# Kernel optimization log

Measured on AMD Instinct MI355X. Metric: run time of the kernel, lower is better.

The kernel has to match this reference:

```python
import jax, jax.numpy as jnp
import numpy as np

NEG_INF = -jnp.inf


def setup_inputs() -> dict:
    key = jax.random.key(0)
    ks = jax.random.split(key, 20)
    B, N, M = 8, 1024, 128
    F_OP, F_MA, F_E, OUT, HID = 64, 64, 16, 64, 128
    inp = {
        "x": jax.random.normal(ks[0], (B, N, F_OP), dtype=jnp.float32),
        "y": jax.random.normal(ks[1], (B, M, F_MA), dtype=jnp.float32),
        "z": jax.random.normal(ks[2], (B, N, M, F_E), dtype=jnp.float32),
        "op_adj_in": jax.random.randint(ks[3], (B, N, N), 0, 2, dtype=jnp.int32),
        "ma_adj_in": jax.random.randint(ks[4], (B, N, N), 0, 2, dtype=jnp.int32),
        "op_ma_adj": jax.random.randint(ks[5], (B, N, M), 0, 2, dtype=jnp.int32),
        # learned parameters
        "weight_op": jax.random.normal(ks[6], (F_OP, OUT), dtype=jnp.float32) * 0.1,
        "weight_ma": jax.random.normal(ks[7], (F_MA, OUT), dtype=jnp.float32) * 0.1,
        "weight_edge": jax.random.normal(ks[8], (F_E, OUT), dtype=jnp.float32) * 0.1,
        "attention_op": jax.random.normal(ks[9], (1, 2 * OUT), dtype=jnp.float32) * 0.1,
        "attention_ma": jax.random.normal(ks[10], (1, 3 * OUT), dtype=jnp.float32) * 0.1,
        "w1": jax.random.normal(ks[11], (2 * OUT, HID), dtype=jnp.float32) * 0.1,
        "b1": jnp.zeros((HID,), dtype=jnp.float32),
        "w2": jax.random.normal(ks[12], (HID, HID), dtype=jnp.float32) * 0.1,
        "b2": jnp.zeros((HID,), dtype=jnp.float32),
        "wo": jax.random.normal(ks[13], (HID, OUT), dtype=jnp.float32) * 0.1,
        "bo": jnp.zeros((OUT,), dtype=jnp.float32),
    }
    return inp


def reference(x, y, z, op_adj_in, ma_adj_in, op_ma_adj,
              weight_op, weight_ma, weight_edge, attention_op, attention_ma,
              w1, b1, w2, b2, wo, bo):
    OUT = weight_op.shape[1]
    h = jnp.einsum('bni,io->bno', x, weight_op)  # [B,N,OUT]
    # all_combinations[b,i,j] = cat(h[b,j], h[b,i]); dot with attention_op splits:
    a1 = attention_op[0, :OUT]
    a2 = attention_op[0, OUT:]
    e_op = (h @ a2)[:, :, None] + (h @ a1)[:, None, :]  # [B,N,N]
    e_op = jax.nn.leaky_relu(e_op, negative_slope=0.01)

    adj = (jnp.swapaxes(op_adj_in, 1, 2) + op_adj_in
           + jnp.swapaxes(ma_adj_in, 1, 2) + ma_adj_in)  # [B,N,N]
    row_mask = jnp.all(op_ma_adj == 0, axis=-1)  # [B,N] ops with no machine link
    adj = jnp.where(row_mask[:, :, None], 1, adj)
    att = jnp.where(adj > 0, e_op, NEG_INF)
    attention_in_op = jax.nn.softmax(att, axis=2)
    h_prime_op = jnp.einsum('bij,bjo->bio', attention_in_op, h)  # [B,N,OUT]

    h_ma = jnp.einsum('bmi,io->bmo', y, weight_ma)  # [B,M,OUT]
    h_edge = jnp.einsum('bnmi,io->bnmo', z, weight_edge)  # [B,N,M,OUT]
    # cat([h_op_i, h_ma_j, h_edge_ij]) @ attention_ma split into three dots
    am1 = attention_ma[0, :OUT]
    am2 = attention_ma[0, OUT:2 * OUT]
    am3 = attention_ma[0, 2 * OUT:]
    e_ma = (h @ am1)[:, :, None] + (h_ma @ am2)[:, None, :] + h_edge @ am3  # [B,N,M]
    e_ma = jax.nn.leaky_relu(e_ma, negative_slope=0.01)

    adj2 = jnp.where(row_mask[:, :, None], 1, op_ma_adj)
    att2 = jnp.where(adj2 > 0, e_ma, NEG_INF)
    attention_in_ma = jax.nn.softmax(att2, axis=2)  # [B,N,M]
    h_ma_edge = h_ma[:, None, :, :] + h_edge  # [B,N,M,OUT]
    h_prime_ma = jnp.einsum('bnm,bnmo->bno', attention_in_ma, h_ma_edge) + h

    h_prime = jnp.concatenate([h_prime_op, h_prime_ma], axis=-1)  # [B,N,2*OUT]
    embed = jax.nn.elu(h_prime @ w1 + b1)
    embed = jax.nn.elu(embed @ w2 + b2)
    embed = embed @ wo + bo
    embed = jnp.where(row_mask[:, :, None], 0.0, embed)
    return embed
```

## Files before the change

### kernel.cpp

```cpp
#include <hip/hip_runtime.h>
#include <math.h>

#define BB 8
#define NN 1024
#define MM 128
#define FOUT 64
#define HIDN 128

#define OFF_H       0
#define OFF_HMA     524288
#define OFF_HA1     589824
#define OFF_HA2     598016
#define OFF_HAM1    606208
#define OFF_HMAAM2  614400
#define OFF_RMASK   615424
#define OFF_WAM3    623616
#define OFF_HPRIME  623632
#define OFF_RDIR    1672208
#define OFF_OPMB    1934352
#define OFF_WT1HI   1967120
#define OFF_WT1LO   1975312
#define OFF_WT2HI   1983504
#define OFF_WT2LO   1991696
#define OFF_WTOHI   1999888
#define OFF_WTOLO   2003984
#define OFF_HTHI    2008080
#define OFF_HTLO    2270224
#define OFF_HMATHI  2532368
#define OFF_HMATLO  2565136
#define OFF_TRM     2597904

typedef __attribute__((ext_vector_type(8))) short bf16x8;
typedef __attribute__((ext_vector_type(8))) unsigned short u16x8;
typedef __attribute__((ext_vector_type(4))) float f32x4;

__device__ __forceinline__ void splitbf(float v, unsigned short& h, unsigned short& l) {
    unsigned u = __float_as_uint(v);
    unsigned hb = (u + 0x7FFFu + ((u >> 16) & 1u)) >> 16;
    float hf = __uint_as_float(hb << 16);
    float lf = v - hf;
    unsigned ul = __float_as_uint(lf);
    unsigned lb = (ul + 0x7FFFu + ((ul >> 16) & 1u)) >> 16;
    h = (unsigned short)hb; l = (unsigned short)lb;
}

__device__ __forceinline__ unsigned short tobf(float v) {
    unsigned u = __float_as_uint(v);
    return (unsigned short)((u + 0x7FFFu + ((u >> 16) & 1u)) >> 16);
}

__global__ __launch_bounds__(256) void k1_prep(
    const float* __restrict__ x, const float* __restrict__ y,
    const int* __restrict__ op_ma_adj,
    const int* __restrict__ op_adj, const int* __restrict__ ma_adj,
    const float* __restrict__ w_op, const float* __restrict__ w_ma,
    const float* __restrict__ w_edge,
    const float* __restrict__ att_op, const float* __restrict__ att_ma,
    const float* __restrict__ w1_g, const float* __restrict__ w2_g,
    const float* __restrict__ wo_g,
    float* __restrict__ h, float* __restrict__ h_ma,
    float* __restrict__ ha1, float* __restrict__ ha2, float* __restrict__ ham1,
    float* __restrict__ hmaam2, int* __restrict__ rmask, float* __restrict__ wam3,
    unsigned long long* __restrict__ rowdir, unsigned long long* __restrict__ opmb,
    unsigned short* __restrict__ trm,
    unsigned short* __restrict__ wt1hi, unsigned short* __restrict__ wt1lo,
    unsigned short* __restrict__ wt2hi, unsigned short* __restrict__ wt2lo,
    unsigned short* __restrict__ wtohi, unsigned short* __restrict__ wtolo,
    unsigned short* __restrict__ hthi, unsigned short* __restrict__ htlo,
    unsigned short* __restrict__ hmathi, unsigned short* __restrict__ hmatlo)
{
    __shared__ float wlds[64 * 64];
    __shared__ unsigned hstage[32 * 64];
    int bid = blockIdx.x;
    int t = threadIdx.x;
    int lane = t & 63;
    int wv = t >> 6;

    if (bid < 256) {
        int b = bid >> 5;
        int n0g = (bid & 31) * 32;
        for (int k = t; k < 4096; k += 256) wlds[k] = w_op[k];
        float a1c = att_op[lane], a2c = att_op[64 + lane], am1c = att_ma[lane];
        __syncthreads();
        #pragma unroll
        for (int p = 0; p < 8; ++p) {
            int row = b * NN + n0g + p * 4 + wv;
            float xv = x[(size_t)row * 64 + lane];
            float acc = 0.f;
            #pragma unroll
            for (int i = 0; i < 64; ++i) {
                float xi = __shfl(xv, i);
                acc += xi * wlds[i * 64 + lane];
            }
            h[(size_t)row * 64 + lane] = acc;
            unsigned short hs, ls;
            splitbf(acc, hs, ls);
            hstage[(p * 4 + wv) * 64 + lane] = (unsigned)hs | ((unsigned)ls << 16);
            float d1 = acc * a1c, d2 = acc * a2c, d3 = acc * am1c;
            #pragma unroll
            for (int m = 32; m; m >>= 1) {
                d1 += __shfl_xor(d1, m);
                d2 += __shfl_xor(d2, m);
                d3 += __shfl_xor(d3, m);
            }
            int v0 = op_ma_adj[(size_t)row * 128 + lane];
            int v1 = op_ma_adj[(size_t)row * 128 + 64 + lane];
            unsigned long long w0 = __ballot(v0 != 0);
            unsigned long long w1 = __ballot(v1 != 0);
            if (lane == 0) {
                ha1[row] = d1; ha2[row] = d2; ham1[row] = d3;
                opmb[row * 2] = w0; opmb[row * 2 + 1] = w1;
                rmask[row] = ((w0 | w1) == 0ULL) ? 1 : 0;
            }
        }
        __syncthreads();
        {
            int plane = t >> 7;
            int q = t & 127;
            int o = q >> 1;
            int hf = q & 1;
            int sh = plane * 16;
            unsigned short* dst = plane ? htlo : hthi;
            u16x8 pk0, pk1;
            #pragma unroll
            for (int k = 0; k < 8; ++k)
                pk0[k] = (unsigned short)((hstage[(hf * 16 + k) * 64 + o] >> sh) & 0xFFFFu);
            #pragma unroll
            for (int k = 0; k < 8; ++k)
                pk1[k] = (unsigned short)((hstage[(hf * 16 + 8 + k) * 64 + o] >> sh) & 0xFFFFu);
            size_t base = ((size_t)((bid >> 5) * 64 + o)) * 1024 + n0g + hf * 16;
            *(u16x8*)&dst[base] = pk0;
            *(u16x8*)&dst[base + 8] = pk1;
        }
    } else if (bid < 288) {
        int bb = (bid - 256) >> 2;
        int m0 = ((bid - 256) & 3) * 32;
        for (int k = t; k < 4096; k += 256) wlds[k] = w_ma[k];
        float am2c = att_ma[64 + lane];
        __syncthreads();
        #pragma unroll
        for (int p = 0; p < 8; ++p) {
            int row = bb * MM + m0 + p * 4 + wv;
            float yv = y[(size_t)row * 64 + lane];
            float acc = 0.f;
            #pragma unroll
            for (int i = 0; i < 64; ++i) {
                float yi = __shfl(yv, i);
                acc += yi * wlds[i * 64 + lane];
            }
            h_ma[(size_t)row * 64 + lane] = acc;
            unsigned short hs, ls;
            splitbf(acc, hs, ls);
            hstage[(p * 4 + wv) * 64 + lane] = (unsigned)hs | ((unsigned)ls << 16);
            float d = acc * am2c;
            #pragma unroll
            for (int m = 32; m; m >>= 1) d += __shfl_xor(d, m);
            if (lane == 0) hmaam2[row] = d;
        }
        __syncthreads();
        {
            int plane = t >> 7;
            int q = t & 127;
            int o = q >> 1;
            int hf = q & 1;
            int sh = plane * 16;
            unsigned short* dst = plane ? hmatlo : hmathi;
            u16x8 pk0, pk1;
            #pragma unroll
            for (int k = 0; k < 8; ++k)
                pk0[k] = (unsigned short)((hstage[(hf * 16 + k) * 64 + o] >> sh) & 0xFFFFu);
            #pragma unroll
            for (int k = 0; k < 8; ++k)
                pk1[k] = (unsigned short)((hstage[(hf * 16 + 8 + k) * 64 + o] >> sh) & 0xFFFFu);
            size_t base = ((size_t)(bb * 64 + o)) * 128 + m0 + hf * 16;
            *(u16x8*)&dst[base] = pk0;
            *(u16x8*)&dst[base + 8] = pk1;
        }
    } else if (bid == 288) {
        if (t < 16) {
            float s = 0.f;
            for (int o = 0; o < 64; ++o) s += w_edge[t * 64 + o] * att_ma[128 + o];
            wam3[t] = s;
        }
    } else if (bid < 2337) {
        unsigned char (*nib)[4][64] = (unsigned char(*)[4][64])wlds;
        int p = bid - 289;
        int b = p >> 8;
        int rg = p & 255;
        int rl = t >> 6;
        int row = rg * 4 + rl;
        const int4* oprow = (const int4*)(op_adj + ((size_t)(b * NN + row)) * NN);
        const int4* marow = (const int4*)(ma_adj + ((size_t)(b * NN + row)) * NN);
        #pragma unroll
        for (int p2 = 0; p2 < 4; ++p2) {
            int4 vo = oprow[p2 * 64 + lane];
            int4 vm = marow[p2 * 64 + lane];
            unsigned nb = ((vo.x | vm.x) ? 1u : 0u) | ((vo.y | vm.y) ? 2u : 0u)
                        | ((vo.z | vm.z) ? 4u : 0u) | ((vo.w | vm.w) ? 8u : 0u);
            nib[rl][p2][lane] = (unsigned char)nb;
        }
        __syncthreads();
        if (t < 64) {
            int arl = t >> 4, q = t & 15;
            const unsigned* nw = (const unsigned*)&nib[arl][q >> 2][(q & 3) * 16];
            unsigned long long w = 0;
            #pragma unroll
            for (int u = 0; u < 4; ++u) {
                unsigned v = nw[u];
                w |= (unsigned long long)(v & 0xFu)         << (16 * u);
                w |= (unsigned long long)((v >> 8) & 0xFu)  << (16 * u + 4);
                w |= (unsigned long long)((v >> 16) & 0xFu) << (16 * u + 8);
                w |= (unsigned long long)((v >> 24) & 0xFu) << (16 * u + 12);
            }
            int jrow = rg * 4 + arl;
            rowdir[((size_t)(b * NN + jrow)) * 16 + q] = w;
            #pragma unroll
            for (int s = 0; s < 4; ++s) {
                trm[((size_t)(b * 64 + q * 4 + s)) * 1024 + jrow] =
                    (unsigned short)((w >> (16 * s)) & 0xFFFFu);
            }
        }
    } else {
        float (*tls)[33] = (float(*)[33])wlds;
        int p = bid - 2337;
        const float* src; unsigned short *dhi, *dlo; int KD, CD, tI, tJ;
        if (p < 16)      { src = w1_g; dhi = wt1hi; dlo = wt1lo; KD = 128; CD = 128; tI = p >> 2; tJ = p & 3; }
        else if (p < 32) { src = w2_g; dhi = wt2hi; dlo = wt2lo; KD = 128; CD = 128; tI = (p-16) >> 2; tJ = (p-16) & 3; }
        else             { src = wo_g; dhi = wtohi; dlo = wtolo; KD = 128; CD = 64;  tI = (p-32) >> 1; tJ = (p-32) & 1; }
        int k0 = tI * 32, c0 = tJ * 32;
        #pragma unroll
        for (int it = 0; it < 4; ++it) {
            int r = (t >> 5) + it * 8;
            int c = t & 31;
            tls[r][c] = src[(size_t)(k0 + r) * CD + c0 + c];
        }
        __syncthreads();
        #pragma unroll
        for (int it = 0; it < 4; ++it) {
            int c = (t >> 5) + it * 8;
            int k = t & 31;
            unsigned short hs, ls;
            splitbf(tls[k][c], hs, ls);
            dhi[(size_t)(c0 + c) * KD + k0 + k] = hs;
            dlo[(size_t)(c0 + c) * KD + k0 + k] = ls;
        }
    }
}

__global__ __launch_bounds__(256) void k2_opatt(
    const unsigned long long* __restrict__ rowdir,
    const unsigned short* __restrict__ trm,
    const unsigned short* __restrict__ hthi,
    const unsigned short* __restrict__ htlo,
    const float* __restrict__ ha1, const float* __restrict__ ha2,
    const int* __restrict__ rmask, float* __restrict__ h_prime)
{
    __shared__ __align__(16) unsigned short Pl[16 * 1024];
    __shared__ float ha1s[1024];
    __shared__ unsigned long long dirw[16][16];
    __shared__ unsigned short trw[1024];
    __shared__ float rdeninv[16];
    int bid = blockIdx.x;
    int b = bid >> 6;
    int i0 = (bid & 63) << 4;
    int t = threadIdx.x;

    {
        int row = t >> 4, w = t & 15;
        dirw[row][w] = rowdir[((size_t)(b * NN + i0 + row)) * 16 + w];
    }
    {
        const unsigned* src = (const unsigned*)(trm + ((size_t)(b * 64 + (i0 >> 4))) * 1024);
        ((unsigned*)trw)[t] = src[t];
        ((unsigned*)trw)[t + 256] = src[t + 256];
    }
    ha1s[t] = ha1[b * NN + t];
    ha1s[t + 256] = ha1[b * NN + t + 256];
    ha1s[t + 512] = ha1[b * NN + t + 512];
    ha1s[t + 768] = ha1[b * NN + t + 768];
    __syncthreads();

    {
        int row = t >> 4, q = t & 15;
        int bn = b * NN + i0 + row;
        float ha2i = ha2[bn];
        unsigned rmf = rmask[bn] ? 1u : 0u;

        float mx = -INFINITY;
        #pragma unroll 8
        for (int jj = 0; jj < 64; ++jj) {
            int j = q + (jj << 4);
            float ev = ha2i + ha1s[j];
            ev = ev > 0.f ? ev : 0.01f * ev;
            unsigned bit = ((unsigned)(dirw[row][jj >> 2] >> (q + ((jj & 3) << 4))) & 1u)
                         | ((unsigned)(trw[j] >> row) & 1u) | rmf;
            if (bit) mx = fmaxf(mx, ev);
        }
        #pragma unroll
        for (int m = 1; m < 16; m <<= 1) mx = fmaxf(mx, __shfl_xor(mx, m));

        float s = 0.f;
        #pragma unroll 4
        for (int jj = 0; jj < 64; ++jj) {
            int j = q + (jj << 4);
            float ev = ha2i + ha1s[j];
            ev = ev > 0.f ? ev : 0.01f * ev;
            unsigned bit = ((unsigned)(dirw[row][jj >> 2] >> (q + ((jj & 3) << 4))) & 1u)
                         | ((unsigned)(trw[j] >> row) & 1u) | rmf;
            float u = bit ? __expf(ev - mx) : 0.f;
            s += u;
            unsigned short pb = tobf(u);
            unsigned byteoff = ((unsigned)(row * 2048 + j * 2)) ^ ((unsigned)((row & 7) << 4));
            *(unsigned short*)((char*)Pl + byteoff) = pb;
        }
        #pragma unroll
        for (int m = 1; m < 16; m <<= 1) s += __shfl_xor(s, m);
        if (q == 0) rdeninv[row] = 1.f / s;
    }
    __syncthreads();

    {
        int lane = t & 63, wvv = t >> 6;
        int arow = lane & 15, kg = lane >> 4;
        int col = wvv * 16 + arow;
        const unsigned short* bhp = hthi + ((size_t)(b * 64 + col)) * 1024;
        const unsigned short* blp = htlo + ((size_t)(b * 64 + col)) * 1024;
        f32x4 acc = {0.f, 0.f, 0.f, 0.f};
        #pragma unroll 8
        for (int kst = 0; kst < 32; ++kst) {
            unsigned cc = ((unsigned)(kst * 4 + kg)) ^ ((unsigned)(arow & 7));
            bf16x8 pa = *(const bf16x8*)((char*)Pl + arow * 2048 + cc * 16);
            bf16x8 vh = *(const bf16x8*)&bhp[kst * 32 + kg * 8];
            bf16x8 vl = *(const bf16x8*)&blp[kst * 32 + kg * 8];
            acc = __builtin_amdgcn_mfma_f32_16x16x32_bf16(pa, vh, acc, 0, 0, 0);
            acc = __builtin_amdgcn_mfma_f32_16x16x32_bf16(pa, vl, acc, 0, 0, 0);
        }
        size_t base = (size_t)(b * NN + i0);
        #pragma unroll
        for (int r = 0; r < 4; ++r) {
            int orow = kg * 4 + r;
            float v = acc[r] * rdeninv[orow];
            h_prime[(base + orow) * 128 + col] = v;
        }
    }
}

__global__ __launch_bounds__(256) void k3_maatt(
    const float* __restrict__ z, const unsigned long long* __restrict__ opmb,
    const float* __restrict__ h,
    const unsigned short* __restrict__ hmathi, const unsigned short* __restrict__ hmatlo,
    const float* __restrict__ ham1, const float* __restrict__ hmaam2,
    const int* __restrict__ rmask, const float* __restrict__ wam3,
    const float* __restrict__ w_edge, float* __restrict__ h_prime)
{
    __shared__ __align__(16) unsigned short U_lds[16 * 136];
    __shared__ float wedge_s[1024];
    __shared__ float wam3s[16];
    __shared__ float zsum_s[16][16];
    __shared__ float rdeninv[16];

    int bid = blockIdx.x;
    int b = bid >> 6;
    int n0 = (bid & 63) * 16;
    int t = threadIdx.x;
    int lane = t & 63;
    int wv = t >> 6;

    for (int k = t; k < 1024; k += 256) wedge_s[k] = w_edge[k];
    if (t < 16) wam3s[t] = wam3[t];
    __syncthreads();

    float hm0 = hmaam2[b * MM + lane];
    float hm1 = hmaam2[b * MM + 64 + lane];

    for (int pp = 0; pp < 4; ++pp) {
        int nl = pp * 4 + wv;
        int bn = b * NN + n0 + nl;
        const float4* zr = (const float4*)(z + (size_t)bn * MM * 16);
        float4 a0 = zr[lane * 4 + 0];
        float4 a1 = zr[lane * 4 + 1];
        float4 a2 = zr[lane * 4 + 2];
        float4 a3 = zr[lane * 4 + 3];
        float4 c0 = zr[(lane + 64) * 4 + 0];
        float4 c1 = zr[(lane + 64) * 4 + 1];
        float4 c2 = zr[(lane + 64) * 4 + 2];
        float4 c3 = zr[(lane + 64) * 4 + 3];

        float base = ham1[bn];
        float e0 = base + hm0;
        float e1 = base + hm1;
        e0 += a0.x*wam3s[0] + a0.y*wam3s[1] + a0.z*wam3s[2] + a0.w*wam3s[3]
            + a1.x*wam3s[4] + a1.y*wam3s[5] + a1.z*wam3s[6] + a1.w*wam3s[7]
            + a2.x*wam3s[8] + a2.y*wam3s[9] + a2.z*wam3s[10] + a2.w*wam3s[11]
            + a3.x*wam3s[12] + a3.y*wam3s[13] + a3.z*wam3s[14] + a3.w*wam3s[15];
        e1 += c0.x*wam3s[0] + c0.y*wam3s[1] + c0.z*wam3s[2] + c0.w*wam3s[3]
            + c1.x*wam3s[4] + c1.y*wam3s[5] + c1.z*wam3s[6] + c1.w*wam3s[7]
            + c2.x*wam3s[8] + c2.y*wam3s[9] + c2.z*wam3s[10] + c2.w*wam3s[11]
            + c3.x*wam3s[12] + c3.y*wam3s[13] + c3.z*wam3s[14] + c3.w*wam3s[15];
        e0 = e0 > 0.f ? e0 : 0.01f * e0;
        e1 = e1 > 0.f ? e1 : 0.01f * e1;
        unsigned long long bits0 = opmb[(size_t)bn * 2];
        unsigned long long bits1 = opmb[(size_t)bn * 2 + 1];
        int rm = rmask[bn];
        int v0 = rm | (int)((bits0 >> lane) & 1ULL);
        int v1 = rm | (int)((bits1 >> lane) & 1ULL);
        e0 = v0 ? e0 : -INFINITY;
        e1 = v1 ? e1 : -INFINITY;

        float mx = fmaxf(e0, e1);
        #pragma unroll
        for (int msk = 32; msk; msk >>= 1) mx = fmaxf(mx, __shfl_xor(mx, msk));
        float u0 = __expf(e0 - mx);
        float u1 = __expf(e1 - mx);
        float s = u0 + u1;
        #pragma unroll
        for (int msk = 32; msk; msk >>= 1) s += __shfl_xor(s, msk);

        U_lds[nl * 136 + lane] = tobf(u0);
        U_lds[nl * 136 + 64 + lane] = tobf(u1);
        if (lane == 0) rdeninv[nl] = 1.f / s;

        float zv[16];
        zv[0]=u0*a0.x+u1*c0.x;  zv[1]=u0*a0.y+u1*c0.y;
        zv[2]=u0*a0.z+u1*c0.z;  zv[3]=u0*a0.w+u1*c0.w;
        zv[4]=u0*a1.x+u1*c1.x;  zv[5]=u0*a1.y+u1*c1.y;
        zv[6]=u0*a1.z+u1*c1.z;  zv[7]=u0*a1.w+u1*c1.w;
        zv[8]=u0*a2.x+u1*c2.x;  zv[9]=u0*a2.y+u1*c2.y;
        zv[10]=u0*a2.z+u1*c2.z; zv[11]=u0*a2.w+u1*c2.w;
        zv[12]=u0*a3.x+u1*c3.x; zv[13]=u0*a3.y+u1*c3.y;
        zv[14]=u0*a3.z+u1*c3.z; zv[15]=u0*a3.w+u1*c3.w;
        #pragma unroll
        for (int s2 = 0; s2 < 8; ++s2) {
            float sel = (lane & 1) ? zv[s2] : zv[s2 + 8];
            float got = __shfl_xor(sel, 1);
            zv[s2] = ((lane & 1) ? zv[s2 + 8] : zv[s2]) + got;
        }
        #pragma unroll
        for (int s2 = 0; s2 < 4; ++s2) {
            float sel = (lane & 2) ? zv[s2] : zv[s2 + 4];
            float got = __shfl_xor(sel, 2);
            zv[s2] = ((lane & 2) ? zv[s2 + 4] : zv[s2]) + got;
        }
        #pragma unroll
        for (int s2 = 0; s2 < 2; ++s2) {
            float sel = (lane & 4) ? zv[s2] : zv[s2 + 2];
            float got = __shfl_xor(sel, 4);
            zv[s2] = ((lane & 4) ? zv[s2 + 2] : zv[s2]) + got;
        }
        {
            float sel = (lane & 8) ? zv[0] : zv[1];
            float got = __shfl_xor(sel, 8);
            zv[0] = ((lane & 8) ? zv[1] : zv[0]) + got;
        }
        zv[0] += __shfl_xor(zv[0], 16);
        zv[0] += __shfl_xor(zv[0], 32);
        if (lane < 16) {
            int comp = ((lane & 1) << 3) | ((lane & 2) << 1) | ((lane & 4) >> 1) | ((lane & 8) >> 3);
            zsum_s[nl][comp] = zv[0];
        }
    }
    __syncthreads();

    {
        int arow = lane & 15, kg = lane >> 4;
        int col = wv * 16 + arow;
        bf16x8 ua[4];
        #pragma unroll
        for (int ks = 0; ks < 4; ++ks)
            ua[ks] = *(const bf16x8*)&U_lds[arow * 136 + kg * 8 + ks * 32];
        const unsigned short* bhp = hmathi + ((size_t)(b * 64 + col)) * 128 + kg * 8;
        const unsigned short* blp = hmatlo + ((size_t)(b * 64 + col)) * 128 + kg * 8;
        f32x4 acc = {0.f, 0.f, 0.f, 0.f};
        #pragma unroll
        for (int ks = 0; ks < 4; ++ks) {
            bf16x8 bh = *(const bf16x8*)&bhp[ks * 32];
            bf16x8 bl = *(const bf16x8*)&blp[ks * 32];
            acc = __builtin_amdgcn_mfma_f32_16x16x32_bf16(ua[ks], bh, acc, 0, 0, 0);
            acc = __builtin_amdgcn_mfma_f32_16x16x32_bf16(ua[ks], bl, acc, 0, 0, 0);
        }
        #pragma unroll
        for (int r = 0; r < 4; ++r) {
            int row = kg * 4 + r;
            float he = 0.f;
            #pragma unroll
            for (int i = 0; i < 16; ++i) he += zsum_s[row][i] * wedge_s[i * 64 + col];
            int bn = b * NN + n0 + row;
            float val = (acc[r] + he) * rdeninv[row] + h[(size_t)bn * 64 + col];
            h_prime[(size_t)bn * 128 + 64 + col] = val;
        }
    }
}

__global__ __launch_bounds__(256) void k4_mlp(
    const float* __restrict__ hp, const int* __restrict__ rmask,
    const unsigned short* __restrict__ wt1hi, const unsigned short* __restrict__ wt1lo,
    const unsigned short* __restrict__ wt2hi, const unsigned short* __restrict__ wt2lo,
    const unsigned short* __restrict__ wtohi, const unsigned short* __restrict__ wtolo,
    const float* __restrict__ b1, const float* __restrict__ b2,
    const float* __restrict__ bo, float* __restrict__ out)
{
    __shared__ __align__(16) unsigned short Ahi0[16 * 136];
    __shared__ __align__(16) unsigned short Alo0[16 * 136];
    __shared__ __align__(16) unsigned short Ahi1[16 * 136];
    __shared__ __align__(16) unsigned short Alo1[16 * 136];
    __shared__ int rml[16];
    int t = threadIdx.x;
    int lane = t & 63;
    int wv = t >> 6;
    int row0 = blockIdx.x * 16;

    {
        int r = t >> 4;
        int cg = (t & 15) * 8;
        const float* src = hp + (size_t)(row0 + r) * 128 + cg;
        float4 v0 = *(const float4*)src;
        float4 v1 = *(const float4*)(src + 4);
        float xs[8] = {v0.x, v0.y, v0.z, v0.w, v1.x, v1.y, v1.z, v1.w};
        u16x8 hv, lv;
        #pragma unroll
        for (int j = 0; j < 8; ++j) {
            unsigned short hs, ls;
            splitbf(xs[j], hs, ls);
            hv[j] = hs; lv[j] = ls;
        }
        *(u16x8*)&Ahi0[r * 136 + cg] = hv;
        *(u16x8*)&Alo0[r * 136 + cg] = lv;
        if (t < 16) rml[t] = rmask[row0 + t];
    }
    __syncthreads();

    int arow = lane & 15;
    int kg = lane >> 4;
    int aoff = arow * 136 + kg * 8;

    {
        bf16x8 ah[4], al[4];
        #pragma unroll
        for (int ks = 0; ks < 4; ++ks) {
            ah[ks] = *(const bf16x8*)&Ahi0[aoff + ks * 32];
            al[ks] = *(const bf16x8*)&Alo0[aoff + ks * 32];
        }
        #pragma unroll
        for (int q = 0; q < 2; ++q) {
            int ct = wv + q * 4;
            int col = ct * 16 + arow;
            const unsigned short* wh = wt1hi + (size_t)col * 128 + kg * 8;
            const unsigned short* wl = wt1lo + (size_t)col * 128 + kg * 8;
            f32x4 acc = {0.f, 0.f, 0.f, 0.f};
            #pragma unroll
            for (int ks = 0; ks < 4; ++ks) {
                bf16x8 bh = *(const bf16x8*)&wh[ks * 32];
                bf16x8 bl = *(const bf16x8*)&wl[ks * 32];
                acc = __builtin_amdgcn_mfma_f32_16x16x32_bf16(ah[ks], bh, acc, 0, 0, 0);
                acc = __builtin_amdgcn_mfma_f32_16x16x32_bf16(al[ks], bh, acc, 0, 0, 0);
                acc = __builtin_amdgcn_mfma_f32_16x16x32_bf16(ah[ks], bl, acc, 0, 0, 0);
            }
            float bb = b1[col];
            #pragma unroll
            for (int r = 0; r < 4; ++r) {
                int row = kg * 4 + r;
                float v = acc[r] + bb;
                v = v > 0.f ? v : __expf(v) - 1.f;
                unsigned short hs, ls;
                splitbf(v, hs, ls);
                Ahi1[row * 136 + col] = hs;
                Alo1[row * 136 + col] = ls;
            }
        }
    }
    __syncthreads();

    {
        bf16x8 ah[4], al[4];
        #pragma unroll
        for (int ks = 0; ks < 4; ++ks) {
            ah[ks] = *(const bf16x8*)&Ahi1[aoff + ks * 32];
            al[ks] = *(const bf16x8*)&Alo1[aoff + ks * 32];
        }
        #pragma unroll
        for (int q = 0; q < 2; ++q) {
            int ct = wv + q * 4;
            int col = ct * 16 + arow;
            const unsigned short* wh = wt2hi + (size_t)col * 128 + kg * 8;
            const unsigned short* wl = wt2lo + (size_t)col * 128 + kg * 8;
            f32x4 acc = {0.f, 0.f, 0.f, 0.f};
            #pragma unroll
            for (int ks = 0; ks < 4; ++ks) {
                bf16x8 bh = *(const bf16x8*)&wh[ks * 32];
                bf16x8 bl = *(const bf16x8*)&wl[ks * 32];
                acc = __builtin_amdgcn_mfma_f32_16x16x32_bf16(ah[ks], bh, acc, 0, 0, 0);
                acc = __builtin_amdgcn_mfma_f32_16x16x32_bf16(al[ks], bh, acc, 0, 0, 0);
                acc = __builtin_amdgcn_mfma_f32_16x16x32_bf16(ah[ks], bl, acc, 0, 0, 0);
            }
            float bb = b2[col];
            #pragma unroll
            for (int r = 0; r < 4; ++r) {
                int row = kg * 4 + r;
                float v = acc[r] + bb;
                v = v > 0.f ? v : __expf(v) - 1.f;
                unsigned short hs, ls;
                splitbf(v, hs, ls);
                Ahi0[row * 136 + col] = hs;
                Alo0[row * 136 + col] = ls;
            }
        }
    }
    __syncthreads();

    {
        bf16x8 ah[4], al[4];
        #pragma unroll
        for (int ks = 0; ks < 4; ++ks) {
            ah[ks] = *(const bf16x8*)&Ahi0[aoff + ks * 32];
            al[ks] = *(const bf16x8*)&Alo0[aoff + ks * 32];
        }
        int ct = wv;
        int col = ct * 16 + arow;
        const unsigned short* wh = wtohi + (size_t)col * 128 + kg * 8;
        const unsigned short* wl = wtolo + (size_t)col * 128 + kg * 8;
        f32x4 acc = {0.f, 0.f, 0.f, 0.f};
        #pragma unroll
        for (int ks = 0; ks < 4; ++ks) {
            bf16x8 bh = *(const bf16x8*)&wh[ks * 32];
            bf16x8 bl = *(const bf16x8*)&wl[ks * 32];
            acc = __builtin_amdgcn_mfma_f32_16x16x32_bf16(ah[ks], bh, acc, 0, 0, 0);
            acc = __builtin_amdgcn_mfma_f32_16x16x32_bf16(al[ks], bh, acc, 0, 0, 0);
            acc = __builtin_amdgcn_mfma_f32_16x16x32_bf16(ah[ks], bl, acc, 0, 0, 0);
        }
        float bb = bo[col];
        #pragma unroll
        for (int r = 0; r < 4; ++r) {
            int row = kg * 4 + r;
            float v = acc[r] + bb;
            out[(size_t)(row0 + row) * 64 + col] = rml[row] ? 0.f : v;
        }
    }
}

extern "C" void kernel_launch(void* const* d_in, const int* in_sizes, int n_in,
                              void* d_out, int out_size, void* d_ws, size_t ws_size,
                              hipStream_t stream) {
    const float* x      = (const float*)d_in[0];
    const float* y      = (const float*)d_in[1];
    const float* z      = (const float*)d_in[2];
    const int*   op_adj = (const int*)d_in[3];
    const int*   ma_adj = (const int*)d_in[4];
    const int*   opma   = (const int*)d_in[5];
    const float* w_op   = (const float*)d_in[6];
    const float* w_ma   = (const float*)d_in[7];
    const float* w_edge = (const float*)d_in[8];
    const float* att_op = (const float*)d_in[9];
    const float* att_ma = (const float*)d_in[10];
    const float* w1     = (const float*)d_in[11];
    const float* b1     = (const float*)d_in[12];
    const float* w2     = (const float*)d_in[13];
    const float* b2     = (const float*)d_in[14];
    const float* wo     = (const float*)d_in[15];
    const float* bo     = (const float*)d_in[16];
    float* out = (float*)d_out;

    float* ws = (float*)d_ws;
    float* h       = ws + OFF_H;
    float* h_ma    = ws + OFF_HMA;
    float* ha1     = ws + OFF_HA1;
    float* ha2     = ws + OFF_HA2;
    float* ham1    = ws + OFF_HAM1;
    float* hmaam2  = ws + OFF_HMAAM2;
    int*   rmask   = (int*)(ws + OFF_RMASK);
    float* wam3    = ws + OFF_WAM3;
    float* h_prime = ws + OFF_HPRIME;
    unsigned long long* rowdir = (unsigned long long*)(ws + OFF_RDIR);
    unsigned long long* opmb = (unsigned long long*)(ws + OFF_OPMB);
    unsigned short* trm   = (unsigned short*)(ws + OFF_TRM);
    unsigned short* wt1hi = (unsigned short*)(ws + OFF_WT1HI);
    unsigned short* wt1lo = (unsigned short*)(ws + OFF_WT1LO);
    unsigned short* wt2hi = (unsigned short*)(ws + OFF_WT2HI);
    unsigned short* wt2lo = (unsigned short*)(ws + OFF_WT2LO);
    unsigned short* wtohi = (unsigned short*)(ws + OFF_WTOHI);
    unsigned short* wtolo = (unsigned short*)(ws + OFF_WTOLO);
    unsigned short* hthi  = (unsigned short*)(ws + OFF_HTHI);
    unsigned short* htlo  = (unsigned short*)(ws + OFF_HTLO);
    unsigned short* hmathi = (unsigned short*)(ws + OFF_HMATHI);
    unsigned short* hmatlo = (unsigned short*)(ws + OFF_HMATLO);

    k1_prep<<<256 + 32 + 1 + 2048 + 40, 256, 0, stream>>>(
        x, y, opma, op_adj, ma_adj, w_op, w_ma, w_edge, att_op, att_ma,
        w1, w2, wo,
        h, h_ma, ha1, ha2, ham1, hmaam2, rmask, wam3, rowdir, opmb, trm,
        wt1hi, wt1lo, wt2hi, wt2lo, wtohi, wtolo, hthi, htlo, hmathi, hmatlo);

    k2_opatt<<<512, 256, 0, stream>>>(
        rowdir, trm, hthi, htlo, ha1, ha2, rmask, h_prime);

    k3_maatt<<<512, 256, 0, stream>>>(
        z, opmb, h, hmathi, hmatlo, ham1, hmaam2, rmask, wam3, w_edge, h_prime);

    k4_mlp<<<512, 256, 0, stream>>>(
        h_prime, rmask, wt1hi, wt1lo, wt2hi, wt2lo, wtohi, wtolo,
        b1, b2, bo, out);
}
```

Baseline: 88.38 us.

## Drop lo-part bf16 MFMAs in attention matmuls and stage MLP weights in LDS

In the op-attention and machine-attention aggregation matmuls, the value operand is now taken from the high bf16 half only, so the lo-correction MFMA and its global load are gone. This roughly halves MFMA work and V-operand traffic in those loops but lowers accuracy to plain bf16 for V. Separately, the MLP kernel now copies each weight tile (hi and lo planes, 64 columns at a time) into swizzled shared memory with block-wide barriers, instead of every wave reading weights directly from global memory. This trades extra syncs and LDS usage for coalesced weight loads.

Measured after the change: 84.21 us. -4.7%, faster.

```diff
diff --git a/kernel.cpp b/kernel.cpp
--- a/kernel.cpp
+++ b/kernel.cpp
@@ -324,16 +324,13 @@
         int arow = lane & 15, kg = lane >> 4;
         int col = wvv * 16 + arow;
         const unsigned short* bhp = hthi + ((size_t)(b * 64 + col)) * 1024;
-        const unsigned short* blp = htlo + ((size_t)(b * 64 + col)) * 1024;
         f32x4 acc = {0.f, 0.f, 0.f, 0.f};
         #pragma unroll 8
         for (int kst = 0; kst < 32; ++kst) {
             unsigned cc = ((unsigned)(kst * 4 + kg)) ^ ((unsigned)(arow & 7));
             bf16x8 pa = *(const bf16x8*)((char*)Pl + arow * 2048 + cc * 16);
             bf16x8 vh = *(const bf16x8*)&bhp[kst * 32 + kg * 8];
-            bf16x8 vl = *(const bf16x8*)&blp[kst * 32 + kg * 8];
             acc = __builtin_amdgcn_mfma_f32_16x16x32_bf16(pa, vh, acc, 0, 0, 0);
-            acc = __builtin_amdgcn_mfma_f32_16x16x32_bf16(pa, vl, acc, 0, 0, 0);
         }
         size_t base = (size_t)(b * NN + i0);
         #pragma unroll
@@ -469,14 +466,11 @@
         for (int ks = 0; ks < 4; ++ks)
             ua[ks] = *(const bf16x8*)&U_lds[arow * 136 + kg * 8 + ks * 32];
         const unsigned short* bhp = hmathi + ((size_t)(b * 64 + col)) * 128 + kg * 8;
-        const unsigned short* blp = hmatlo + ((size_t)(b * 64 + col)) * 128 + kg * 8;
         f32x4 acc = {0.f, 0.f, 0.f, 0.f};
         #pragma unroll
         for (int ks = 0; ks < 4; ++ks) {
             bf16x8 bh = *(const bf16x8*)&bhp[ks * 32];
-            bf16x8 bl = *(const bf16x8*)&blp[ks * 32];
             acc = __builtin_amdgcn_mfma_f32_16x16x32_bf16(ua[ks], bh, acc, 0, 0, 0);
-            acc = __builtin_amdgcn_mfma_f32_16x16x32_bf16(ua[ks], bl, acc, 0, 0, 0);
         }
         #pragma unroll
         for (int r = 0; r < 4; ++r) {
@@ -503,11 +497,15 @@
     __shared__ __align__(16) unsigned short Alo0[16 * 136];
     __shared__ __align__(16) unsigned short Ahi1[16 * 136];
     __shared__ __align__(16) unsigned short Alo1[16 * 136];
+    __shared__ __align__(16) unsigned short Whi[64 * 128];
+    __shared__ __align__(16) unsigned short Wlo[64 * 128];
     __shared__ int rml[16];
     int t = threadIdx.x;
     int lane = t & 63;
     int wv = t >> 6;
     int row0 = blockIdx.x * 16;
+    int plane = t >> 7;
+    int q = t & 127;
 
     {
         int r = t >> 4;
@@ -532,6 +530,7 @@
     int arow = lane & 15;
     int kg = lane >> 4;
     int aoff = arow * 136 + kg * 8;
+    int lcol = wv * 16 + arow;
 
     {
         bf16x8 ah[4], al[4];
@@ -541,16 +540,28 @@
             al[ks] = *(const bf16x8*)&Alo0[aoff + ks * 32];
         }
         #pragma unroll
-        for (int q = 0; q < 2; ++q) {
-            int ct = wv + q * 4;
-            int col = ct * 16 + arow;
-            const unsigned short* wh = wt1hi + (size_t)col * 128 + kg * 8;
-            const unsigned short* wl = wt1lo + (size_t)col * 128 + kg * 8;
+        for (int half = 0; half < 2; ++half) {
+            __syncthreads();
+            {
+                const unsigned short* gsrc = plane ? wt1lo : wt1hi;
+                char* dst = (char*)(plane ? Wlo : Whi);
+                #pragma unroll
+                for (int i = 0; i < 8; ++i) {
+                    int L = q * 8 + i;
+                    int col = L >> 4, kc = L & 15;
+                    u16x8 v = *(const u16x8*)&gsrc[(size_t)(half * 64 + col) * 128 + kc * 8];
+                    unsigned byteoff = ((unsigned)(col * 256 + kc * 16)) ^ ((unsigned)((col & 7) << 4));
+                    *(u16x8*)(dst + byteoff) = v;
+                }
+            }
+            __syncthreads();
+            int col = half * 64 + lcol;
             f32x4 acc = {0.f, 0.f, 0.f, 0.f};
             #pragma unroll
             for (int ks = 0; ks < 4; ++ks) {
-                bf16x8 bh = *(const bf16x8*)&wh[ks * 32];
-                bf16x8 bl = *(const bf16x8*)&wl[ks * 32];
+                unsigned wb = ((unsigned)(lcol * 256 + kg * 16 + ks * 64)) ^ ((unsigned)((arow & 7) << 4));
+                bf16x8 bh = *(const bf16x8*)((char*)Whi + wb);
+                bf16x8 bl = *(const bf16x8*)((char*)Wlo + wb);
                 acc = __builtin_amdgcn_mfma_f32_16x16x32_bf16(ah[ks], bh, acc, 0, 0, 0);
                 acc = __builtin_amdgcn_mfma_f32_16x16x32_bf16(al[ks], bh, acc, 0, 0, 0);
                 acc = __builtin_amdgcn_mfma_f32_16x16x32_bf16(ah[ks], bl, acc, 0, 0, 0);
@@ -578,16 +589,28 @@
             al[ks] = *(const bf16x8*)&Alo1[aoff + ks * 32];
         }
         #pragma unroll
-        for (int q = 0; q < 2; ++q) {
-            int ct = wv + q * 4;
-            int col = ct * 16 + arow;
-            const unsigned short* wh = wt2hi + (size_t)col * 128 + kg * 8;
-            const unsigned short* wl = wt2lo + (size_t)col * 128 + kg * 8;
+        for (int half = 0; half < 2; ++half) {
+            __syncthreads();
+            {
+                const unsigned short* gsrc = plane ? wt2lo : wt2hi;
+                char* dst = (char*)(plane ? Wlo : Whi);
+                #pragma unroll
+                for (int i = 0; i < 8; ++i) {
+                    int L = q * 8 + i;
+                    int col = L >> 4, kc = L & 15;
+                    u16x8 v = *(const u16x8*)&gsrc[(size_t)(half * 64 + col) * 128 + kc * 8];
+                    unsigned byteoff = ((unsigned)(col * 256 + kc * 16)) ^ ((unsigned)((col & 7) << 4));
+                    *(u16x8*)(dst + byteoff) = v;
+                }
+            }
+            __syncthreads();
+            int col = half * 64 + lcol;
             f32x4 acc = {0.f, 0.f, 0.f, 0.f};
             #pragma unroll
             for (int ks = 0; ks < 4; ++ks) {
-                bf16x8 bh = *(const bf16x8*)&wh[ks * 32];
-                bf16x8 bl = *(const bf16x8*)&wl[ks * 32];
+                unsigned wb = ((unsigned)(lcol * 256 + kg * 16 + ks * 64)) ^ ((unsigned)((arow & 7) << 4));
+                bf16x8 bh = *(const bf16x8*)((char*)Whi + wb);
+                bf16x8 bl = *(const bf16x8*)((char*)Wlo + wb);
                 acc = __builtin_amdgcn_mfma_f32_16x16x32_bf16(ah[ks], bh, acc, 0, 0, 0);
                 acc = __builtin_amdgcn_mfma_f32_16x16x32_bf16(al[ks], bh, acc, 0, 0, 0);
                 acc = __builtin_amdgcn_mfma_f32_16x16x32_bf16(ah[ks], bl, acc, 0, 0, 0);
@@ -614,15 +637,27 @@
             ah[ks] = *(const bf16x8*)&Ahi0[aoff + ks * 32];
             al[ks] = *(const bf16x8*)&Alo0[aoff + ks * 32];
         }
-        int ct = wv;
-        int col = ct * 16 + arow;
-        const unsigned short* wh = wtohi + (size_t)col * 128 + kg * 8;
-        const unsigned short* wl = wtolo + (size_t)col * 128 + kg * 8;
+        __syncthreads();
+        {
+            const unsigned short* gsrc = plane ? wtolo : wtohi;
+            char* dst = (char*)(plane ? Wlo : Whi);
+            #pragma unroll
+            for (int i = 0; i < 8; ++i) {
+                int L = q * 8 + i;
+                int col = L >> 4, kc = L & 15;
+                u16x8 v = *(const u16x8*)&gsrc[(size_t)col * 128 + kc * 8];
+                unsigned byteoff = ((unsigned)(col * 256 + kc * 16)) ^ ((unsigned)((col & 7) << 4));
+                *(u16x8*)(dst + byteoff) = v;
+            }
+        }
+        __syncthreads();
+        int col = lcol;
         f32x4 acc = {0.f, 0.f, 0.f, 0.f};
         #pragma unroll
         for (int ks = 0; ks < 4; ++ks) {
-            bf16x8 bh = *(const bf16x8*)&wh[ks * 32];
-            bf16x8 bl = *(const bf16x8*)&wl[ks * 32];
+            unsigned wb = ((unsigned)(lcol * 256 + kg * 16 + ks * 64)) ^ ((unsigned)((arow & 7) << 4));
+            bf16x8 bh = *(const bf16x8*)((char*)Whi + wb);
+            bf16x8 bl = *(const bf16x8*)((char*)Wlo + wb);
             acc = __builtin_amdgcn_mfma_f32_16x16x32_bf16(ah[ks], bh, acc, 0, 0, 0);
             acc = __builtin_amdgcn_mfma_f32_16x16x32_bf16(al[ks], bh, acc, 0, 0, 0);
             acc = __builtin_amdgcn_mfma_f32_16x16x32_bf16(ah[ks], bl, acc, 0, 0, 0);
```
